# Kernel tuning notes

Measured on AMD Instinct MI355X. Metric: run time of the kernel, lower is better.

## Reference

```python
import jax, jax.numpy as jnp
import numpy as np

N = 100000
E = 1600000
IN = 256
H = 4
D = 32      # n_hidden per head
C = 47      # n_classes
NEG_SLOPE = 0.2


def setup_inputs() -> dict:
    key = jax.random.key(0)
    ks = jax.random.split(key, 16)
    s = 0.1
    inp = {
        "x": jax.random.normal(ks[0], (N, IN), dtype=jnp.float32),
        "src": jax.random.randint(ks[1], (E,), 0, N),
        "dst": jax.random.randint(ks[2], (E,), 0, N),
        # layer 1: IN -> H*D
        "W1": jax.random.normal(ks[3], (IN, H * D), dtype=jnp.float32) * s,
        "al1": jax.random.normal(ks[4], (H, D), dtype=jnp.float32) * s,
        "ar1": jax.random.normal(ks[5], (H, D), dtype=jnp.float32) * s,
        "b1": jnp.zeros((H * D,), dtype=jnp.float32),
        # layer 2: H*D -> H*D
        "W2": jax.random.normal(ks[6], (H * D, H * D), dtype=jnp.float32) * s,
        "al2": jax.random.normal(ks[7], (H, D), dtype=jnp.float32) * s,
        "ar2": jax.random.normal(ks[8], (H, D), dtype=jnp.float32) * s,
        "b2": jnp.zeros((H * D,), dtype=jnp.float32),
        # layer 3: H*D -> H*C
        "W3": jax.random.normal(ks[9], (H * D, H * C), dtype=jnp.float32) * s,
        "al3": jax.random.normal(ks[10], (H, C), dtype=jnp.float32) * s,
        "ar3": jax.random.normal(ks[11], (H, C), dtype=jnp.float32) * s,
        "b3": jnp.zeros((H * C,), dtype=jnp.float32),
    }
    return inp


def gat_conv(h, W, al, ar, b, src, dst, out_dim, activate):
    # h: [N, F_in] -> feat: [N, H, out_dim]
    feat = (h @ W).reshape(N, H, out_dim)
    el = jnp.sum(feat * al[None], axis=-1)          # [N, H]
    er = jnp.sum(feat * ar[None], axis=-1)          # [N, H]
    e = jax.nn.leaky_relu(el[src] + er[dst], NEG_SLOPE)  # [E, H]
    # edge softmax per destination node (segment softmax)
    m = jax.ops.segment_max(e, dst, num_segments=N)      # [N, H]
    ex = jnp.exp(e - m[dst])                             # [E, H]
    den = jax.ops.segment_sum(ex, dst, num_segments=N)   # [N, H]
    alpha = ex / den[dst]                                # [E, H]
    # scatter-weighted aggregation: sum_e alpha_e * feat[src_e]
    out = jax.ops.segment_sum(feat[src] * alpha[:, :, None], dst, num_segments=N)
    out = out + b.reshape(1, H, out_dim)
    return jax.nn.relu(out) if activate else out


def reference(x, src, dst, W1, al1, ar1, b1, W2, al2, ar2, b2, W3, al3, ar3, b3):
    h = gat_conv(x, W1, al1, ar1, b1, src, dst, D, True).reshape(N, H * D)
    h = gat_conv(h, W2, al2, ar2, b2, src, dst, D, True).reshape(N, H * D)
    h = gat_conv(h, W3, al3, ar3, b3, src, dst, C, False)  # [N, H, C]
    h = h.mean(axis=1)                                     # head mean
    return jax.nn.log_softmax(h, axis=-1)
```

## Files before the change

kernel.cpp:

```cpp
#include <hip/hip_runtime.h>
#include <hip/hip_bf16.h>

typedef unsigned short ushort;
typedef unsigned int uint;
typedef __attribute__((ext_vector_type(8))) short short8;
typedef __attribute__((ext_vector_type(4))) float floatx4;

#define NEG_SLOPE 0.2f

__device__ __forceinline__ float bu2f(ushort u) {
  uint t = ((uint)u) << 16;
  return __uint_as_float(t);
}
__device__ __forceinline__ ushort f2bu(float f) {
  __hip_bfloat16 h = __float2bfloat16(f);
  return *(ushort*)&h;
}
__device__ __forceinline__ float lo2f(uint u) { return __uint_as_float(u << 16); }
__device__ __forceinline__ float hi2f(uint u) { return __uint_as_float(u & 0xffff0000u); }
__device__ __forceinline__ float lrelu(float e) { return (e > 0.f) ? e : NEG_SLOPE * e; }

__global__ void zero_int_kernel(int* __restrict__ p, int n) {
  int i = blockIdx.x * blockDim.x + threadIdx.x;
  if (i < n) p[i] = 0;
}

__global__ void hist_kernel(const int* __restrict__ dst, int* __restrict__ deg, int E) {
  int e = blockIdx.x * blockDim.x + threadIdx.x;
  if (e < E) atomicAdd(&deg[dst[e]], 1);
}

__global__ void scan1_kernel(const int* __restrict__ deg, int* __restrict__ part,
                             int* __restrict__ bsums, int n) {
  __shared__ int sdata[256];
  int t = threadIdx.x;
  int base = blockIdx.x * 1024;
  int v[4]; int s = 0;
#pragma unroll
  for (int j = 0; j < 4; ++j) {
    int idx = base + t * 4 + j;
    v[j] = (idx < n) ? deg[idx] : 0;
    s += v[j];
  }
  sdata[t] = s;
  __syncthreads();
  for (int off = 1; off < 256; off <<= 1) {
    int x = 0;
    if (t >= off) x = sdata[t - off];
    __syncthreads();
    if (t >= off) sdata[t] += x;
    __syncthreads();
  }
  if (t == 255) bsums[blockIdx.x] = sdata[255];
  int run = (t > 0) ? sdata[t - 1] : 0;
#pragma unroll
  for (int j = 0; j < 4; ++j) {
    int idx = base + t * 4 + j;
    if (idx < n) part[idx] = run;
    run += v[j];
  }
}

__global__ void scan2_kernel(int* __restrict__ bsums, int nb) {
  __shared__ int sdata[256];
  int t = threadIdx.x;
  sdata[t] = (t < nb) ? bsums[t] : 0;
  __syncthreads();
  for (int off = 1; off < 256; off <<= 1) {
    int x = 0;
    if (t >= off) x = sdata[t - off];
    __syncthreads();
    if (t >= off) sdata[t] += x;
    __syncthreads();
  }
  if (t < nb) bsums[t] = (t > 0) ? sdata[t - 1] : 0;
}

__global__ void scan3_kernel(const int* __restrict__ part, const int* __restrict__ bsums,
                             int* __restrict__ rowptr, int* __restrict__ cursor,
                             int n, int Etot) {
  int i = blockIdx.x * blockDim.x + threadIdx.x;
  if (i < n) {
    int v = part[i] + bsums[i >> 10];
    rowptr[i] = v;
    cursor[i] = v;
  }
  if (i == 0) rowptr[n] = Etot;
}

__global__ void scatter_kernel(const int* __restrict__ src, const int* __restrict__ dst,
                               int* __restrict__ cursor, int* __restrict__ csr_src, int E) {
  int e = blockIdx.x * blockDim.x + threadIdx.x;
  if (e < E) {
    int pos = atomicAdd(&cursor[dst[e]], 1);
    csr_src[pos] = src[e];
  }
}

__global__ void splitx_kernel(const float* __restrict__ x, ushort* __restrict__ xhi,
                              ushort* __restrict__ xlo, int n) {
  int base = (blockIdx.x * blockDim.x + threadIdx.x) * 4;
  if (base >= n) return;
  float4 a = *(const float4*)(x + base);
  float v[4] = {a.x, a.y, a.z, a.w};
  ushort hi[4], lo[4];
#pragma unroll
  for (int j = 0; j < 4; ++j) {
    hi[j] = f2bu(v[j]);
    lo[j] = f2bu(v[j] - bu2f(hi[j]));
  }
  uint2 ho, loo;
  ho.x = (uint)hi[0] | ((uint)hi[1] << 16);
  ho.y = (uint)hi[2] | ((uint)hi[3] << 16);
  loo.x = (uint)lo[0] | ((uint)lo[1] << 16);
  loo.y = (uint)lo[2] | ((uint)lo[3] << 16);
  *(uint2*)(xhi + base) = ho;
  *(uint2*)(xlo + base) = loo;
}

__global__ void splitW_kernel(const float* __restrict__ W, ushort* __restrict__ WtH,
                              ushort* __restrict__ WtL, int K, int Nc) {
  int idx = blockIdx.x * blockDim.x + threadIdx.x;
  if (idx >= K * Nc) return;
  int n = idx / K, k = idx - n * K;
  float w = W[(size_t)k * Nc + n];
  ushort hi = f2bu(w);
  WtH[idx] = hi;
  WtL[idx] = f2bu(w - bu2f(hi));
}

#define GBM 128
#define GBN 64
#define GBK 32
#define SA 40

__global__ __launch_bounds__(256) void gemm_split_kernel(
    const ushort* __restrict__ Ah, const ushort* __restrict__ Al,
    const ushort* __restrict__ Bh, const ushort* __restrict__ Bl,
    ushort* __restrict__ C, int M, int K, int Nc) {
  __shared__ ushort AsH[GBM * SA];
  __shared__ ushort AsL[GBM * SA];
  __shared__ ushort BsH[GBN * SA];
  __shared__ ushort BsL[GBN * SA];
  int tid = threadIdx.x;
  int lane = tid & 63;
  int wave = tid >> 6;
  int wm = wave & 1, wn = wave >> 1;
  int rowBase = blockIdx.y * GBM;
  int colBase = blockIdx.x * GBN;
  int q = lane >> 4;
  int ln = lane & 15;

  floatx4 acc[4][2] = {};

  for (int k0 = 0; k0 < K; k0 += GBK) {
#pragma unroll
    for (int it = 0; it < 2; ++it) {
      int i = tid + it * 256;
      int r = i >> 2, seg = i & 3;
      int grow = rowBase + r;
      uint4 vh = {0u, 0u, 0u, 0u}, vl = {0u, 0u, 0u, 0u};
      if (grow < M) {
        size_t off = (size_t)grow * K + k0 + seg * 8;
        vh = *(const uint4*)(Ah + off);
        vl = *(const uint4*)(Al + off);
      }
      *(uint4*)&AsH[r * SA + seg * 8] = vh;
      *(uint4*)&AsL[r * SA + seg * 8] = vl;
    }
    {
      int n = tid >> 2, seg = tid & 3;
      int gcol = colBase + n;
      uint4 vh = {0u, 0u, 0u, 0u}, vl = {0u, 0u, 0u, 0u};
      if (gcol < Nc) {
        size_t off = (size_t)gcol * K + k0 + seg * 8;
        vh = *(const uint4*)(Bh + off);
        vl = *(const uint4*)(Bl + off);
      }
      *(uint4*)&BsH[n * SA + seg * 8] = vh;
      *(uint4*)&BsL[n * SA + seg * 8] = vl;
    }
    __syncthreads();
    short8 afH[4], afL[4], bfH[2], bfL[2];
#pragma unroll
    for (int mt = 0; mt < 4; ++mt) {
      int r = (wm * 64 + mt * 16 + ln) * SA + q * 8;
      afH[mt] = *(const short8*)&AsH[r];
      afL[mt] = *(const short8*)&AsL[r];
    }
#pragma unroll
    for (int nt = 0; nt < 2; ++nt) {
      int r = (wn * 32 + nt * 16 + ln) * SA + q * 8;
      bfH[nt] = *(const short8*)&BsH[r];
      bfL[nt] = *(const short8*)&BsL[r];
    }
#pragma unroll
    for (int mt = 0; mt < 4; ++mt)
#pragma unroll
      for (int nt = 0; nt < 2; ++nt) {
        acc[mt][nt] = __builtin_amdgcn_mfma_f32_16x16x32_bf16(afH[mt], bfH[nt], acc[mt][nt], 0, 0, 0);
        acc[mt][nt] = __builtin_amdgcn_mfma_f32_16x16x32_bf16(afH[mt], bfL[nt], acc[mt][nt], 0, 0, 0);
        acc[mt][nt] = __builtin_amdgcn_mfma_f32_16x16x32_bf16(afL[mt], bfH[nt], acc[mt][nt], 0, 0, 0);
      }
    __syncthreads();
  }
#pragma unroll
  for (int mt = 0; mt < 4; ++mt) {
#pragma unroll
    for (int nt = 0; nt < 2; ++nt) {
      int col = colBase + wn * 32 + nt * 16 + ln;
      if (col < Nc) {
#pragma unroll
        for (int r = 0; r < 4; ++r) {
          int row = rowBase + wm * 64 + mt * 16 + q * 4 + r;
          if (row < M) C[(size_t)row * Nc + col] = f2bu(acc[mt][nt][r]);
        }
      }
    }
  }
}

__global__ void elr128_kernel(const ushort* __restrict__ feat, const float* __restrict__ al,
                              const float* __restrict__ ar, float* __restrict__ el,
                              float* __restrict__ er, int N) {
  int g = blockIdx.x * blockDim.x + threadIdx.x;
  if (g >= N * 4) return;
  int n = g >> 2, h = g & 3;
  const uint4* fp = (const uint4*)(feat + (size_t)n * 128 + h * 32);
  const float* alp = al + h * 32;
  const float* arp = ar + h * 32;
  float sl = 0.f, sr = 0.f;
#pragma unroll
  for (int b = 0; b < 4; ++b) {
    uint4 u = fp[b];
    uint w[4] = {u.x, u.y, u.z, u.w};
#pragma unroll
    for (int j = 0; j < 4; ++j) {
      int d = b * 8 + j * 2;
      float f0 = lo2f(w[j]), f1 = hi2f(w[j]);
      sl += f0 * alp[d] + f1 * alp[d + 1];
      sr += f0 * arp[d] + f1 * arp[d + 1];
    }
  }
  el[g] = sl;
  er[g] = sr;
}

__global__ void elr3_kernel(const ushort* __restrict__ feat, const float* __restrict__ al,
                            const float* __restrict__ ar, float* __restrict__ el,
                            float* __restrict__ er, int N) {
  int g = blockIdx.x * blockDim.x + threadIdx.x;
  if (g >= N * 4) return;
  int n = g >> 2, h = g & 3;
  const ushort* fp = feat + (size_t)n * 188 + h * 47;
  float sl = 0.f, sr = 0.f;
  for (int d = 0; d < 47; ++d) {
    float f = bu2f(fp[d]);
    sl += f * al[h * 47 + d];
    sr += f * ar[h * 47 + d];
  }
  el[g] = sl;
  er[g] = sr;
}

__global__ __launch_bounds__(256) void agg128_kernel(
    const int* __restrict__ rowptr, const int* __restrict__ csr_src,
    const ushort* __restrict__ feat, const float* __restrict__ el,
    const float* __restrict__ er, const float* __restrict__ bias,
    ushort* __restrict__ hhi, ushort* __restrict__ hlo, int N) {
  int lane = threadIdx.x & 63;
  int v = blockIdx.x * 4 + (threadIdx.x >> 6);
  if (v >= N) return;
  float4 er4 = *(const float4*)(er + (size_t)v * 4);
  int r0 = rowptr[v], r1 = rowptr[v + 1];
  int hh = lane & 3;
  float eh = (hh == 0) ? er4.x : (hh == 1) ? er4.y : (hh == 2) ? er4.z : er4.w;
  int hf = lane >> 4;
  const uint* fb = (const uint*)feat;
  float a0 = 0.f, a1 = 0.f, den = 0.f;
  for (int i0 = r0; i0 < r1; i0 += 16) {
    int i = i0 + (lane >> 2);
    int sv = 0;
    float xv = 0.f;
    if (i < r1) {
      sv = csr_src[i];
      xv = __expf(lrelu(el[(size_t)sv * 4 + hh] + eh));
    }
    int cnt = r1 - i0;
    if (cnt > 16) cnt = 16;
    for (int j = 0; j < cnt; ++j) {
      int s = __shfl(sv, j * 4);
      float x = __shfl(xv, j * 4 + hf);
      uint u = fb[(size_t)s * 64 + lane];
      den += x;
      a0 += x * lo2f(u);
      a1 += x * hi2f(u);
    }
  }
  float o0 = (den > 0.f) ? a0 / den : 0.f;
  float o1 = (den > 0.f) ? a1 / den : 0.f;
  o0 = fmaxf(o0 + bias[2 * lane], 0.f);
  o1 = fmaxf(o1 + bias[2 * lane + 1], 0.f);
  ushort h0 = f2bu(o0), h1 = f2bu(o1);
  ushort l0 = f2bu(o0 - bu2f(h0)), l1 = f2bu(o1 - bu2f(h1));
  ((uint*)hhi)[(size_t)v * 64 + lane] = (uint)h0 | ((uint)h1 << 16);
  ((uint*)hlo)[(size_t)v * 64 + lane] = (uint)l0 | ((uint)l1 << 16);
}

__global__ __launch_bounds__(256) void agg3_kernel(
    const int* __restrict__ rowptr, const int* __restrict__ csr_src,
    const ushort* __restrict__ feat, const float* __restrict__ el,
    const float* __restrict__ er, const float* __restrict__ bias,
    float* __restrict__ out, int N) {
  __shared__ float svm[4][188];
  int lane = threadIdx.x & 63;
  int w = threadIdx.x >> 6;
  int v = blockIdx.x * 4 + w;
  bool valid = (v < N);
  float4 er4 = {0.f, 0.f, 0.f, 0.f};
  int r0 = 0, r1 = 0;
  if (valid) {
    er4 = *(const float4*)(er + (size_t)v * 4);
    r0 = rowptr[v];
    r1 = rowptr[v + 1];
  }
  int hh = lane & 3;
  float eh = (hh == 0) ? er4.x : (hh == 1) ? er4.y : (hh == 2) ? er4.z : er4.w;
  int fa = 2 * lane, fbi = 2 * lane + 1;
  int fc = 128 + 2 * lane, fd = 129 + 2 * lane;
  bool hasC = (fd < 188);
  int ha = fa / 47, hb = fbi / 47;
  int hc = hasC ? fc / 47 : 3, hd = hasC ? fd / 47 : 3;
  const uint* fpb = (const uint*)feat;
  float aa = 0.f, ab = 0.f, ac = 0.f, ad = 0.f;
  float da = 0.f, db = 0.f, dc = 0.f, dd = 0.f;
  for (int i0 = r0; i0 < r1; i0 += 16) {
    int i = i0 + (lane >> 2);
    int sv = 0;
    float xv = 0.f;
    if (i < r1) {
      sv = csr_src[i];
      xv = __expf(lrelu(el[(size_t)sv * 4 + hh] + eh));
    }
    int cnt = r1 - i0;
    if (cnt > 16) cnt = 16;
    for (int j = 0; j < cnt; ++j) {
      int s = __shfl(sv, j * 4);
      float xa = __shfl(xv, j * 4 + ha);
      float xb = __shfl(xv, j * 4 + hb);
      uint u0 = fpb[(size_t)s * 94 + lane];
      da += xa; db += xb;
      aa += xa * lo2f(u0);
      ab += xb * hi2f(u0);
      if (hasC) {
        float xc = __shfl(xv, j * 4 + hc);
        float xd = __shfl(xv, j * 4 + hd);
        uint u1 = fpb[(size_t)s * 94 + 64 + lane];
        dc += xc; dd += xd;
        ac += xc * lo2f(u1);
        ad += xd * hi2f(u1);
      }
    }
  }
  float oa = ((da > 0.f) ? aa / da : 0.f) + bias[fa];
  float ob = ((db > 0.f) ? ab / db : 0.f) + bias[fbi];
  if (valid) {
    svm[w][fa] = oa;
    svm[w][fbi] = ob;
    if (hasC) {
      float oc = ((dc > 0.f) ? ac / dc : 0.f) + bias[fc];
      float od = ((dd > 0.f) ? ad / dd : 0.f) + bias[fd];
      svm[w][fc] = oc;
      svm[w][fd] = od;
    }
  }
  __syncthreads();
  float val = -1e30f;
  if (valid && lane < 47)
    val = 0.25f * (svm[w][lane] + svm[w][47 + lane] + svm[w][94 + lane] + svm[w][141 + lane]);
  float mx = val;
#pragma unroll
  for (int off = 32; off > 0; off >>= 1) mx = fmaxf(mx, __shfl_xor(mx, off));
  float ex = (lane < 47) ? __expf(val - mx) : 0.f;
  float sum = ex;
#pragma unroll
  for (int off = 32; off > 0; off >>= 1) sum += __shfl_xor(sum, off);
  float res = val - mx - logf(sum);
  if (valid && lane < 47) out[(size_t)v * 47 + lane] = res;
}

extern "C" void kernel_launch(void* const* d_in, const int* in_sizes, int n_in,
                              void* d_out, int out_size, void* d_ws, size_t ws_size,
                              hipStream_t stream) {
  const int N = 100000, E = 1600000, IN = 256;
  const int F = 128;
  const int F3 = 188;

  const float* x = (const float*)d_in[0];
  const int* src = (const int*)d_in[1];
  const int* dst = (const int*)d_in[2];
  const float* W1 = (const float*)d_in[3];
  const float* al1 = (const float*)d_in[4];
  const float* ar1 = (const float*)d_in[5];
  const float* b1 = (const float*)d_in[6];
  const float* W2 = (const float*)d_in[7];
  const float* al2 = (const float*)d_in[8];
  const float* ar2 = (const float*)d_in[9];
  const float* b2 = (const float*)d_in[10];
  const float* W3 = (const float*)d_in[11];
  const float* al3 = (const float*)d_in[12];
  const float* ar3 = (const float*)d_in[13];
  const float* b3 = (const float*)d_in[14];

  char* p = (char*)d_ws;
  auto alloc = [&](size_t bytes) -> char* {
    char* r = p;
    p += (bytes + 255) & ~(size_t)255;
    return r;
  };
  ushort* xhi = (ushort*)alloc((size_t)N * IN * sizeof(ushort));
  ushort* xlo = (ushort*)alloc((size_t)N * IN * sizeof(ushort));
  ushort* feat = (ushort*)alloc((size_t)N * F3 * sizeof(ushort));
  ushort* Wt1h = (ushort*)alloc((size_t)F * IN * sizeof(ushort));
  ushort* Wt1l = (ushort*)alloc((size_t)F * IN * sizeof(ushort));
  ushort* Wt2h = (ushort*)alloc((size_t)F * F * sizeof(ushort));
  ushort* Wt2l = (ushort*)alloc((size_t)F * F * sizeof(ushort));
  ushort* Wt3h = (ushort*)alloc((size_t)F3 * F * sizeof(ushort));
  ushort* Wt3l = (ushort*)alloc((size_t)F3 * F * sizeof(ushort));
  float* el = (float*)alloc((size_t)N * 4 * sizeof(float));
  float* er = (float*)alloc((size_t)N * 4 * sizeof(float));
  int* deg = (int*)alloc((size_t)N * sizeof(int));
  int* part = (int*)alloc((size_t)N * sizeof(int));
  int* bsums = (int*)alloc(256 * sizeof(int));
  int* rowptr = (int*)alloc((size_t)(N + 1) * sizeof(int));
  int* cursor = (int*)alloc((size_t)N * sizeof(int));
  int* csr_src = (int*)alloc((size_t)E * sizeof(int));

  ushort* hhi = xhi;
  ushort* hlo = xlo;

  zero_int_kernel<<<(N + 255) / 256, 256, 0, stream>>>(deg, N);
  hist_kernel<<<(E + 255) / 256, 256, 0, stream>>>(dst, deg, E);
  int nb = (N + 1023) / 1024;
  scan1_kernel<<<nb, 256, 0, stream>>>(deg, part, bsums, N);
  scan2_kernel<<<1, 256, 0, stream>>>(bsums, nb);
  scan3_kernel<<<(N + 255) / 256, 256, 0, stream>>>(part, bsums, rowptr, cursor, N, E);
  scatter_kernel<<<(E + 255) / 256, 256, 0, stream>>>(src, dst, cursor, csr_src, E);

  splitx_kernel<<<(N * IN / 4 + 255) / 256, 256, 0, stream>>>(x, xhi, xlo, N * IN);
  splitW_kernel<<<(IN * F + 255) / 256, 256, 0, stream>>>(W1, Wt1h, Wt1l, IN, F);
  splitW_kernel<<<(F * F + 255) / 256, 256, 0, stream>>>(W2, Wt2h, Wt2l, F, F);
  splitW_kernel<<<(F * F3 + 255) / 256, 256, 0, stream>>>(W3, Wt3h, Wt3l, F, F3);

  int rowBlocks = (N + GBM - 1) / GBM;
  int nodeBlocks = (N + 3) / 4;

  gemm_split_kernel<<<dim3(F / GBN, rowBlocks), 256, 0, stream>>>(
      xhi, xlo, Wt1h, Wt1l, feat, N, IN, F);
  elr128_kernel<<<(N * 4 + 255) / 256, 256, 0, stream>>>(feat, al1, ar1, el, er, N);
  agg128_kernel<<<nodeBlocks, 256, 0, stream>>>(rowptr, csr_src, feat, el, er, b1, hhi, hlo, N);

  gemm_split_kernel<<<dim3(F / GBN, rowBlocks), 256, 0, stream>>>(
      hhi, hlo, Wt2h, Wt2l, feat, N, F, F);
  elr128_kernel<<<(N * 4 + 255) / 256, 256, 0, stream>>>(feat, al2, ar2, el, er, N);
  agg128_kernel<<<nodeBlocks, 256, 0, stream>>>(rowptr, csr_src, feat, el, er, b2, hhi, hlo, N);

  gemm_split_kernel<<<dim3((F3 + GBN - 1) / GBN, rowBlocks), 256, 0, stream>>>(
      hhi, hlo, Wt3h, Wt3l, feat, N, F, F3);
  elr3_kernel<<<(N * 4 + 255) / 256, 256, 0, stream>>>(feat, al3, ar3, el, er, N);
  agg3_kernel<<<nodeBlocks, 256, 0, stream>>>(rowptr, csr_src, feat, el, er, b3,
                                              (float*)d_out, N);
}
```

Before: 995.2 us.

## Precompute edge softmax weights in separate kernel before aggregation

```diff
diff --git a/kernel.cpp b/kernel.cpp
--- a/kernel.cpp
+++ b/kernel.cpp
@@ -263,42 +263,55 @@
   er[g] = sr;
 }
 
+__global__ __launch_bounds__(256) void edgew_kernel(
+    const int* __restrict__ rowptr, const int* __restrict__ csr_src,
+    const float* __restrict__ el, const float* __restrict__ er,
+    float* __restrict__ wbuf, float* __restrict__ den, int N) {
+  int lane = threadIdx.x & 63;
+  int v = blockIdx.x * 4 + (threadIdx.x >> 6);
+  if (v >= N) return;
+  int hh = lane & 3;
+  float eh = er[(size_t)v * 4 + hh];
+  int r0 = rowptr[v], r1 = rowptr[v + 1];
+  float dsum = 0.f;
+  for (int i0 = r0; i0 < r1; i0 += 16) {
+    int i = i0 + (lane >> 2);
+    if (i < r1) {
+      int sv = csr_src[i];
+      float w = __expf(lrelu(el[(size_t)sv * 4 + hh] + eh));
+      wbuf[(size_t)i * 4 + hh] = w;
+      dsum += w;
+    }
+  }
+#pragma unroll
+  for (int off = 4; off < 64; off <<= 1) dsum += __shfl_xor(dsum, off);
+  if (lane < 4) den[(size_t)v * 4 + hh] = dsum;
+}
+
 __global__ __launch_bounds__(256) void agg128_kernel(
     const int* __restrict__ rowptr, const int* __restrict__ csr_src,
-    const ushort* __restrict__ feat, const float* __restrict__ el,
-    const float* __restrict__ er, const float* __restrict__ bias,
+    const ushort* __restrict__ feat, const float* __restrict__ wbuf,
+    const float* __restrict__ den, const float* __restrict__ bias,
     ushort* __restrict__ hhi, ushort* __restrict__ hlo, int N) {
   int lane = threadIdx.x & 63;
   int v = blockIdx.x * 4 + (threadIdx.x >> 6);
   if (v >= N) return;
-  float4 er4 = *(const float4*)(er + (size_t)v * 4);
   int r0 = rowptr[v], r1 = rowptr[v + 1];
-  int hh = lane & 3;
-  float eh = (hh == 0) ? er4.x : (hh == 1) ? er4.y : (hh == 2) ? er4.z : er4.w;
   int hf = lane >> 4;
   const uint* fb = (const uint*)feat;
-  float a0 = 0.f, a1 = 0.f, den = 0.f;
-  for (int i0 = r0; i0 < r1; i0 += 16) {
-    int i = i0 + (lane >> 2);
-    int sv = 0;
-    float xv = 0.f;
-    if (i < r1) {
-      sv = csr_src[i];
-      xv = __expf(lrelu(el[(size_t)sv * 4 + hh] + eh));
-    }
-    int cnt = r1 - i0;
-    if (cnt > 16) cnt = 16;
-    for (int j = 0; j < cnt; ++j) {
-      int s = __shfl(sv, j * 4);
-      float x = __shfl(xv, j * 4 + hf);
-      uint u = fb[(size_t)s * 64 + lane];
-      den += x;
-      a0 += x * lo2f(u);
-      a1 += x * hi2f(u);
-    }
-  }
-  float o0 = (den > 0.f) ? a0 / den : 0.f;
-  float o1 = (den > 0.f) ? a1 / den : 0.f;
+  float a0 = 0.f, a1 = 0.f;
+#pragma unroll 2
+  for (int i = r0; i < r1; ++i) {
+    int s = __builtin_amdgcn_readfirstlane(csr_src[i]);
+    float x = wbuf[(size_t)i * 4 + hf];
+    const uint* fr = fb + ((size_t)s << 6);
+    uint u = fr[lane];
+    a0 = fmaf(x, lo2f(u), a0);
+    a1 = fmaf(x, hi2f(u), a1);
+  }
+  float d = den[(size_t)v * 4 + hf];
+  float o0 = (d > 0.f) ? a0 / d : 0.f;
+  float o1 = (d > 0.f) ? a1 / d : 0.f;
   o0 = fmaxf(o0 + bias[2 * lane], 0.f);
   o1 = fmaxf(o1 + bias[2 * lane + 1], 0.f);
   ushort h0 = f2bu(o0), h1 = f2bu(o1);
@@ -309,23 +322,19 @@
 
 __global__ __launch_bounds__(256) void agg3_kernel(
     const int* __restrict__ rowptr, const int* __restrict__ csr_src,
-    const ushort* __restrict__ feat, const float* __restrict__ el,
-    const float* __restrict__ er, const float* __restrict__ bias,
+    const ushort* __restrict__ feat, const float* __restrict__ wbuf,
+    const float* __restrict__ den, const float* __restrict__ bias,
     float* __restrict__ out, int N) {
   __shared__ float svm[4][188];
   int lane = threadIdx.x & 63;
   int w = threadIdx.x >> 6;
   int v = blockIdx.x * 4 + w;
   bool valid = (v < N);
-  float4 er4 = {0.f, 0.f, 0.f, 0.f};
   int r0 = 0, r1 = 0;
   if (valid) {
-    er4 = *(const float4*)(er + (size_t)v * 4);
     r0 = rowptr[v];
     r1 = rowptr[v + 1];
   }
-  int hh = lane & 3;
-  float eh = (hh == 0) ? er4.x : (hh == 1) ? er4.y : (hh == 2) ? er4.z : er4.w;
   int fa = 2 * lane, fbi = 2 * lane + 1;
   int fc = 128 + 2 * lane, fd = 129 + 2 * lane;
   bool hasC = (fd < 188);
@@ -333,33 +342,30 @@
   int hc = hasC ? fc / 47 : 3, hd = hasC ? fd / 47 : 3;
   const uint* fpb = (const uint*)feat;
   float aa = 0.f, ab = 0.f, ac = 0.f, ad = 0.f;
-  float da = 0.f, db = 0.f, dc = 0.f, dd = 0.f;
-  for (int i0 = r0; i0 < r1; i0 += 16) {
-    int i = i0 + (lane >> 2);
-    int sv = 0;
-    float xv = 0.f;
-    if (i < r1) {
-      sv = csr_src[i];
-      xv = __expf(lrelu(el[(size_t)sv * 4 + hh] + eh));
-    }
-    int cnt = r1 - i0;
-    if (cnt > 16) cnt = 16;
-    for (int j = 0; j < cnt; ++j) {
-      int s = __shfl(sv, j * 4);
-      float xa = __shfl(xv, j * 4 + ha);
-      float xb = __shfl(xv, j * 4 + hb);
-      uint u0 = fpb[(size_t)s * 94 + lane];
-      da += xa; db += xb;
-      aa += xa * lo2f(u0);
-      ab += xb * hi2f(u0);
-      if (hasC) {
-        float xc = __shfl(xv, j * 4 + hc);
-        float xd = __shfl(xv, j * 4 + hd);
-        uint u1 = fpb[(size_t)s * 94 + 64 + lane];
-        dc += xc; dd += xd;
-        ac += xc * lo2f(u1);
-        ad += xd * hi2f(u1);
-      }
+#pragma unroll 2
+  for (int i = r0; i < r1; ++i) {
+    int s = __builtin_amdgcn_readfirstlane(csr_src[i]);
+    const float* wp = wbuf + (size_t)i * 4;
+    float xa = wp[ha], xb = wp[hb];
+    const uint* fr = fpb + (size_t)s * 94;
+    uint u0 = fr[lane];
+    aa = fmaf(xa, lo2f(u0), aa);
+    ab = fmaf(xb, hi2f(u0), ab);
+    if (hasC) {
+      float xc = wp[hc], xd = wp[hd];
+      uint u1 = fr[64 + lane];
+      ac = fmaf(xc, lo2f(u1), ac);
+      ad = fmaf(xd, hi2f(u1), ad);
+    }
+  }
+  float da = 0.f, db = 0.f, dc = 1.f, dd = 1.f;
+  if (valid) {
+    const float* dp = den + (size_t)v * 4;
+    da = dp[ha];
+    db = dp[hb];
+    if (hasC) {
+      dc = dp[hc];
+      dd = dp[hd];
     }
   }
   float oa = ((da > 0.f) ? aa / da : 0.f) + bias[fa];
@@ -435,6 +441,8 @@
   int* rowptr = (int*)alloc((size_t)(N + 1) * sizeof(int));
   int* cursor = (int*)alloc((size_t)N * sizeof(int));
   int* csr_src = (int*)alloc((size_t)E * sizeof(int));
+  float* wbuf = (float*)alloc((size_t)E * 4 * sizeof(float));
+  float* den = (float*)alloc((size_t)N * 4 * sizeof(float));
 
   ushort* hhi = xhi;
   ushort* hlo = xlo;
@@ -458,16 +466,19 @@
   gemm_split_kernel<<<dim3(F / GBN, rowBlocks), 256, 0, stream>>>(
       xhi, xlo, Wt1h, Wt1l, feat, N, IN, F);
   elr128_kernel<<<(N * 4 + 255) / 256, 256, 0, stream>>>(feat, al1, ar1, el, er, N);
-  agg128_kernel<<<nodeBlocks, 256, 0, stream>>>(rowptr, csr_src, feat, el, er, b1, hhi, hlo, N);
+  edgew_kernel<<<nodeBlocks, 256, 0, stream>>>(rowptr, csr_src, el, er, wbuf, den, N);
+  agg128_kernel<<<nodeBlocks, 256, 0, stream>>>(rowptr, csr_src, feat, wbuf, den, b1, hhi, hlo, N);
 
   gemm_split_kernel<<<dim3(F / GBN, rowBlocks), 256, 0, stream>>>(
       hhi, hlo, Wt2h, Wt2l, feat, N, F, F);
   elr128_kernel<<<(N * 4 + 255) / 256, 256, 0, stream>>>(feat, al2, ar2, el, er, N);
-  agg128_kernel<<<nodeBlocks, 256, 0, stream>>>(rowptr, csr_src, feat, el, er, b2, hhi, hlo, N);
+  edgew_kernel<<<nodeBlocks, 256, 0, stream>>>(rowptr, csr_src, el, er, wbuf, den, N);
+  agg128_kernel<<<nodeBlocks, 256, 0, stream>>>(rowptr, csr_src, feat, wbuf, den, b2, hhi, hlo, N);
 
   gemm_split_kernel<<<dim3((F3 + GBN - 1) / GBN, rowBlocks), 256, 0, stream>>>(
       hhi, hlo, Wt3h, Wt3l, feat, N, F, F3);
   elr3_kernel<<<(N * 4 + 255) / 256, 256, 0, stream>>>(feat, al3, ar3, el, er, N);
-  agg3_kernel<<<nodeBlocks, 256, 0, stream>>>(rowptr, csr_src, feat, el, er, b3,
+  edgew_kernel<<<nodeBlocks, 256, 0, stream>>>(rowptr, csr_src, el, er, wbuf, den, N);
+  agg3_kernel<<<nodeBlocks, 256, 0, stream>>>(rowptr, csr_src, feat, wbuf, den, b3,
                                               (float*)d_out, N);
 }
```

Result: slower. 1.179 ms (+18.5%).
